# Kernel optimization log

Measured on AMD Instinct MI355X. Metric: run time of the kernel, lower is better.

## Reference

```python
import jax, jax.numpy as jnp
import numpy as np

MESSAGE_PASSES = 3  # constants.message_passes
F_NODE = 64   # hidden_node_features
F_EDGE = 16   # n_edge_features
M_MSG = 64    # message_size
OUT_DIM = 128
B, N = 8, 256
EDGE_DENSITY = 0.1


def setup_inputs() -> dict:
    key = jax.random.key(0)
    ks = jax.random.split(key, 12)
    nodes = jax.random.normal(ks[0], (B, N, F_NODE), dtype=jnp.float32)
    # sparse positive edge features: rand * bernoulli connectivity (avg degree ~ N*density)
    raw = jax.random.uniform(ks[1], (B, N, N, F_EDGE), dtype=jnp.float32)
    conn = (jax.random.uniform(ks[2], (B, N, N)) < EDGE_DENSITY).astype(jnp.float32)
    edges = raw * conn[..., None]
    s = 0.05
    return {
        "nodes": nodes,
        "edges": edges,
        # message MLP: cat(neighbour, edge) -> message_size
        "W_msg": jax.random.normal(ks[3], (F_NODE + F_EDGE, M_MSG), dtype=jnp.float32) * s,
        "b_msg": jnp.zeros((M_MSG,), dtype=jnp.float32),
        # GRU cell (input=message_size, hidden=F_NODE), gates [r|z|n]
        "W_i": jax.random.normal(ks[4], (M_MSG, 3 * F_NODE), dtype=jnp.float32) * s,
        "W_h": jax.random.normal(ks[5], (F_NODE, 3 * F_NODE), dtype=jnp.float32) * s,
        "b_i": jnp.zeros((3 * F_NODE,), dtype=jnp.float32),
        "b_h": jnp.zeros((3 * F_NODE,), dtype=jnp.float32),
        # gated readout
        "W_g": jax.random.normal(ks[6], (2 * F_NODE, OUT_DIM), dtype=jnp.float32) * s,
        "b_g": jnp.zeros((OUT_DIM,), dtype=jnp.float32),
        "W_e": jax.random.normal(ks[7], (F_NODE, OUT_DIM), dtype=jnp.float32) * s,
        "b_e": jnp.zeros((OUT_DIM,), dtype=jnp.float32),
    }


def reference(nodes, edges, W_msg, b_msg, W_i, W_h, b_i, b_h, W_g, b_g, W_e, b_e):
    # adjacency[b,i,j] != 0  <=>  edge (i<-j) exists (original: edges.sum(3).nonzero)
    adjacency = edges.sum(axis=-1)                                   # (B,N,N)
    nbr_mask = (adjacency != 0).astype(nodes.dtype)                  # (B,N,N)
    node_mask = (adjacency.sum(axis=-1) != 0)                        # (B,N) bool
    node_mask_f = node_mask.astype(nodes.dtype)

    h = nodes                                                        # hidden_nodes init = nodes
    b, n, f = nodes.shape
    for _ in range(MESSAGE_PASSES):
        # message_terms over all (node i, neighbour j) pairs; masked sum == padded-gather sum
        nghb = jnp.broadcast_to(h[:, None, :, :], (b, n, n, f))      # (B,N,N,F) neighbour feats
        feat = jnp.concatenate([nghb, edges], axis=-1)               # (B,N,N,F+E)
        terms = jax.nn.relu(feat @ W_msg + b_msg)                    # (B,N,N,M)
        messages = jnp.einsum('bijm,bij->bim', terms, nbr_mask)      # summation aggregation
        # GRU cell update
        gi = messages @ W_i + b_i                                    # (B,N,3F)
        gh = h @ W_h + b_h
        ir, iz, inn = jnp.split(gi, 3, axis=-1)
        hr, hz, hn = jnp.split(gh, 3, axis=-1)
        r = jax.nn.sigmoid(ir + hr)
        z = jax.nn.sigmoid(iz + hz)
        ng = jnp.tanh(inn + r * hn)
        h_new = (1.0 - z) * ng + z * h
        # only nodes with nonzero degree are scattered back (original indexes node_batch idc)
        h = jnp.where(node_mask[..., None], h_new, h)

    # gated readout: sum_i mask_i * sigmoid(g([h_i, x_i])) * e(h_i)
    gate = jax.nn.sigmoid(jnp.concatenate([h, nodes], axis=-1) @ W_g + b_g)  # (B,N,OUT)
    emb = h @ W_e + b_e                                                      # (B,N,OUT)
    out = jnp.einsum('bno,bn->bo', gate * emb, node_mask_f)                  # (B,OUT)
    return out
```

## Files before the change

kernel.cpp:

```cpp
#include <hip/hip_runtime.h>
#include <hip/hip_bf16.h>

#define BB 8
#define NN 256
#define FF 64
#define EE 16
#define MM 64
#define G3 192
#define OUTD 128
#define ROWS (BB*NN)
#define MAXD 64

__global__ __launch_bounds__(256) void k_prep(
    const float* __restrict__ nodes, const float* __restrict__ edges,
    const float* __restrict__ Wmsg, const float* __restrict__ bmsg,
    int* __restrict__ deg, int* __restrict__ nbr,
    float* __restrict__ h, float* __restrict__ hn)
{
    int row = blockIdx.x;
    int tid = threadIdx.x;
    __shared__ int cnt;
    __shared__ float snode[FF];
    if (tid == 0) cnt = 0;
    __syncthreads();

    const float4* ep = (const float4*)(edges + (((size_t)row) * NN + tid) * EE);
    float4 a = ep[0], b4 = ep[1], c4 = ep[2], d4 = ep[3];
    float s = a.x + a.y + a.z + a.w + b4.x + b4.y + b4.z + b4.w
            + c4.x + c4.y + c4.z + c4.w + d4.x + d4.y + d4.z + d4.w;
    if (s != 0.0f) {
        int slot = atomicAdd(&cnt, 1);
        if (slot < MAXD) nbr[row * MAXD + slot] = tid;
    }
    if (tid < FF) snode[tid] = nodes[(size_t)row * FF + tid];
    __syncthreads();

    if (tid == 0) deg[row] = (cnt < MAXD) ? cnt : MAXD;
    if (tid < FF) h[row * FF + tid] = snode[tid];
    if (tid < MM) {
        float acc = bmsg[tid];
        #pragma unroll 8
        for (int k = 0; k < FF; ++k) acc += snode[k] * Wmsg[k * MM + tid];
        hn[row * MM + tid] = acc;
    }
}

#define MSG_WAVES 4
__global__ __launch_bounds__(256) void k_msg(
    const float* __restrict__ edges, const float* __restrict__ Wmsg,
    const int* __restrict__ deg, const int* __restrict__ nbr,
    const float* __restrict__ hn, float* __restrict__ msg)
{
    int row = blockIdx.x;
    int b   = row >> 8;
    int tid = threadIdx.x;
    int w   = tid >> 6;
    int t   = tid & 63;

    float we[EE];
    #pragma unroll
    for (int k = 0; k < EE; ++k) we[k] = Wmsg[(FF + k) * MM + t];

    __shared__ float efeat[MAXD][EE];
    __shared__ float part[MSG_WAVES][MM];

    int d = deg[row];
    for (int s4 = tid; s4 < d * EE; s4 += 256) {
        int slot = s4 >> 4, k = s4 & 15;
        int j = nbr[row * MAXD + slot];
        efeat[slot][k] = edges[(((size_t)row) * NN + j) * EE + k];
    }
    __syncthreads();

    float acc = 0.0f;
    for (int s = w; s < d; s += MSG_WAVES) {
        int j = nbr[row * MAXD + s];
        float term = hn[(((size_t)b) * NN + j) * MM + t];
        #pragma unroll
        for (int k = 0; k < EE; ++k) term += efeat[s][k] * we[k];
        acc += fmaxf(term, 0.0f);
    }
    part[w][t] = acc;
    __syncthreads();
    if (w == 0) {
        msg[row * MM + t] = part[0][t] + part[1][t] + part[2][t] + part[3][t];
    }
}

#define GRU_NODES 8
__global__ __launch_bounds__(512) void k_gru(
    const float* __restrict__ Wi, const float* __restrict__ Wh,
    const float* __restrict__ bi, const float* __restrict__ bh,
    const float* __restrict__ Wmsg, const float* __restrict__ bmsg,
    const int* __restrict__ deg,
    const float* __restrict__ msg, float* __restrict__ h, float* __restrict__ hn,
    int last)
{
    int g = threadIdx.x >> 6;
    int t = threadIdx.x & 63;
    int row = blockIdx.x * GRU_NODES + g;

    __shared__ float sm[GRU_NODES][FF];
    __shared__ float sh[GRU_NODES][FF];
    sm[g][t] = msg[row * MM + t];
    sh[g][t] = h[row * FF + t];
    __syncthreads();

    float ir = bi[t], iz = bi[64 + t], in_ = bi[128 + t];
    float hr = bh[t], hz = bh[64 + t], hn_ = bh[128 + t];
    #pragma unroll 4
    for (int k = 0; k < FF; ++k) {
        float mk = sm[g][k], hk = sh[g][k];
        ir  += mk * Wi[k * G3 + t];
        iz  += mk * Wi[k * G3 + 64 + t];
        in_ += mk * Wi[k * G3 + 128 + t];
        hr  += hk * Wh[k * G3 + t];
        hz  += hk * Wh[k * G3 + 64 + t];
        hn_ += hk * Wh[k * G3 + 128 + t];
    }
    float r  = 1.0f / (1.0f + __expf(-(ir + hr)));
    float z  = 1.0f / (1.0f + __expf(-(iz + hz)));
    float ng = tanhf(in_ + r * hn_);
    float hold = sh[g][t];
    float hnew = (1.0f - z) * ng + z * hold;
    if (deg[row] == 0) hnew = hold;
    h[row * FF + t] = hnew;

    __syncthreads();
    sh[g][t] = hnew;
    __syncthreads();

    if (!last) {
        float acc = bmsg[t];
        #pragma unroll 8
        for (int k = 0; k < FF; ++k) acc += sh[g][k] * Wmsg[k * MM + t];
        hn[row * MM + t] = acc;
    }
}

#define RO_NODES 8
__global__ __launch_bounds__(1024) void k_readout(
    const float* __restrict__ nodes, const float* __restrict__ Wg,
    const float* __restrict__ bg, const float* __restrict__ We,
    const float* __restrict__ be, const int* __restrict__ deg,
    const float* __restrict__ h, float* __restrict__ out)
{
    int g = threadIdx.x >> 7;
    int o = threadIdx.x & 127;
    int row = blockIdx.x * RO_NODES + g;
    int b   = row >> 8;

    __shared__ float sh[RO_NODES][FF];
    __shared__ float sx[RO_NODES][FF];
    __shared__ float red[RO_NODES][OUTD];
    if (o < FF) {
        sh[g][o] = h[row * FF + o];
        sx[g][o] = nodes[(size_t)row * FF + o];
    }
    __syncthreads();

    float gacc = bg[o], eacc = be[o];
    #pragma unroll 4
    for (int k = 0; k < FF; ++k) {
        float hk = sh[g][k];
        gacc += hk * Wg[k * OUTD + o];
        eacc += hk * We[k * OUTD + o];
    }
    #pragma unroll 4
    for (int k = 0; k < FF; ++k) gacc += sx[g][k] * Wg[(FF + k) * OUTD + o];

    float val = (deg[row] != 0) ? (1.0f / (1.0f + __expf(-gacc))) * eacc : 0.0f;
    red[g][o] = val;
    __syncthreads();
    if (g == 0) {
        float s = 0.0f;
        #pragma unroll
        for (int q = 0; q < RO_NODES; ++q) s += red[q][o];
        atomicAdd(&out[b * OUTD + o], s);
    }
}

extern "C" void kernel_launch(void* const* d_in, const int* in_sizes, int n_in,
                              void* d_out, int out_size, void* d_ws, size_t ws_size,
                              hipStream_t stream) {
    const float* nodes = (const float*)d_in[0];
    const float* edges = (const float*)d_in[1];
    const float* Wmsg  = (const float*)d_in[2];
    const float* bmsg  = (const float*)d_in[3];
    const float* Wi    = (const float*)d_in[4];
    const float* Wh    = (const float*)d_in[5];
    const float* bi    = (const float*)d_in[6];
    const float* bh    = (const float*)d_in[7];
    const float* Wg    = (const float*)d_in[8];
    const float* bg    = (const float*)d_in[9];
    const float* We    = (const float*)d_in[10];
    const float* be    = (const float*)d_in[11];
    float* out = (float*)d_out;

    char* ws = (char*)d_ws;
    int*   deg = (int*)ws;
    int*   nbr = (int*)(ws + 8192);
    float* h   = (float*)(ws + 8192 + ROWS * MAXD * 4);
    float* hn  = h + ROWS * FF;
    float* msg = hn + ROWS * MM;

    hipMemsetAsync(d_out, 0, (size_t)BB * OUTD * sizeof(float), stream);

    k_prep<<<ROWS, 256, 0, stream>>>(nodes, edges, Wmsg, bmsg, deg, nbr, h, hn);

    for (int p = 0; p < 3; ++p) {
        k_msg<<<ROWS, 256, 0, stream>>>(edges, Wmsg, deg, nbr, hn, msg);
        k_gru<<<ROWS / GRU_NODES, 64 * GRU_NODES, 0, stream>>>(
            Wi, Wh, bi, bh, Wmsg, bmsg, deg, msg, h, hn, (p == 2) ? 1 : 0);
    }

    k_readout<<<ROWS / RO_NODES, 128 * RO_NODES, 0, stream>>>(
        nodes, Wg, bg, We, be, deg, h, out);
}
```

Measured before the change: 166.8 us.

## Fuse message, GRU, projection and readout into one per-pass kernel

Merges the message aggregation, GRU update, next-pass neighbour projection and, on the last pass, the gated readout into a single kernel per pass, with one block per node. This cuts the launch count from eight to four, removes the msg round trip through global memory, and ping-pongs hn between two buffers to avoid read/write hazards across nodes. The neighbour-list build now uses wave ballot and popcount instead of shared atomics, which also makes the neighbour order deterministic. In exchange, the GRU and readout math run one node per block, so the weight matrices are reloaded per node and only part of each 256-thread block is busy during those phases.

```diff
diff --git a/kernel.cpp b/kernel.cpp
--- a/kernel.cpp
+++ b/kernel.cpp
@@ -11,6 +11,10 @@
 #define ROWS (BB*NN)
 #define MAXD 64
 
+__device__ __forceinline__ float sigmoidf_(float x) {
+    return 1.0f / (1.0f + __expf(-x));
+}
+
 __global__ __launch_bounds__(256) void k_prep(
     const float* __restrict__ nodes, const float* __restrict__ edges,
     const float* __restrict__ Wmsg, const float* __restrict__ bmsg,
@@ -19,23 +23,30 @@
 {
     int row = blockIdx.x;
     int tid = threadIdx.x;
-    __shared__ int cnt;
+    int lane = tid & 63, wv = tid >> 6;
+    __shared__ int wcnt[4];
     __shared__ float snode[FF];
-    if (tid == 0) cnt = 0;
-    __syncthreads();
 
     const float4* ep = (const float4*)(edges + (((size_t)row) * NN + tid) * EE);
     float4 a = ep[0], b4 = ep[1], c4 = ep[2], d4 = ep[3];
     float s = a.x + a.y + a.z + a.w + b4.x + b4.y + b4.z + b4.w
             + c4.x + c4.y + c4.z + c4.w + d4.x + d4.y + d4.z + d4.w;
-    if (s != 0.0f) {
-        int slot = atomicAdd(&cnt, 1);
-        if (slot < MAXD) nbr[row * MAXD + slot] = tid;
-    }
+    bool pred = (s != 0.0f);
+    unsigned long long m = __ballot(pred);
+    if (lane == 0) wcnt[wv] = __popcll(m);
     if (tid < FF) snode[tid] = nodes[(size_t)row * FF + tid];
     __syncthreads();
 
-    if (tid == 0) deg[row] = (cnt < MAXD) ? cnt : MAXD;
+    int base = 0;
+    #pragma unroll
+    for (int q = 0; q < 4; ++q) base += (q < wv) ? wcnt[q] : 0;
+    int slot = base + __popcll(m & ((1ull << lane) - 1ull));
+    if (pred && slot < MAXD) nbr[row * MAXD + slot] = tid;
+
+    if (tid == 0) {
+        int tot = wcnt[0] + wcnt[1] + wcnt[2] + wcnt[3];
+        deg[row] = (tot < MAXD) ? tot : MAXD;
+    }
     if (tid < FF) h[row * FF + tid] = snode[tid];
     if (tid < MM) {
         float acc = bmsg[tid];
@@ -45,138 +56,115 @@
     }
 }
 
-#define MSG_WAVES 4
-__global__ __launch_bounds__(256) void k_msg(
-    const float* __restrict__ edges, const float* __restrict__ Wmsg,
+__global__ __launch_bounds__(256) void k_pass(
+    const float* __restrict__ edges,
+    const float* __restrict__ Wmsg, const float* __restrict__ bmsg,
+    const float* __restrict__ Wi, const float* __restrict__ Wh,
+    const float* __restrict__ bi, const float* __restrict__ bh,
+    const float* __restrict__ nodes,
+    const float* __restrict__ Wg, const float* __restrict__ bg,
+    const float* __restrict__ We, const float* __restrict__ be,
     const int* __restrict__ deg, const int* __restrict__ nbr,
-    const float* __restrict__ hn, float* __restrict__ msg)
+    const float* __restrict__ hn_in, float* __restrict__ hn_out,
+    float* __restrict__ h, float* __restrict__ out, int last)
 {
-    int row = blockIdx.x;
-    int b   = row >> 8;
+    int row = blockIdx.x, b = row >> 8;
     int tid = threadIdx.x;
-    int w   = tid >> 6;
-    int t   = tid & 63;
+    int w = tid >> 6, t = tid & 63;
+
+    __shared__ int   snbr[MAXD];
+    __shared__ float efeat[MAXD][EE];
+    __shared__ float part[4][MM];
+    __shared__ float smsg[MM];
+    __shared__ float shold[FF];
+    __shared__ float sx[FF];
+    __shared__ float gI[3][FF], gH[3][FF];
+    __shared__ float shnew[FF];
+    __shared__ float eo[OUTD];
+
+    int d = deg[row];
+    if (tid < d)  snbr[tid]  = nbr[row * MAXD + tid];
+    if (tid < FF) shold[tid] = h[row * FF + tid];
+    if (last && tid < FF) sx[tid] = nodes[(size_t)row * FF + tid];
 
     float we[EE];
     #pragma unroll
     for (int k = 0; k < EE; ++k) we[k] = Wmsg[(FF + k) * MM + t];
-
-    __shared__ float efeat[MAXD][EE];
-    __shared__ float part[MSG_WAVES][MM];
-
-    int d = deg[row];
+    __syncthreads();
+
     for (int s4 = tid; s4 < d * EE; s4 += 256) {
         int slot = s4 >> 4, k = s4 & 15;
-        int j = nbr[row * MAXD + slot];
-        efeat[slot][k] = edges[(((size_t)row) * NN + j) * EE + k];
+        efeat[slot][k] = edges[(((size_t)row) * NN + snbr[slot]) * EE + k];
     }
     __syncthreads();
 
     float acc = 0.0f;
-    for (int s = w; s < d; s += MSG_WAVES) {
-        int j = nbr[row * MAXD + s];
-        float term = hn[(((size_t)b) * NN + j) * MM + t];
+    for (int s = w; s < d; s += 4) {
+        int j = snbr[s];
+        float term = hn_in[(((size_t)b) * NN + j) * MM + t];
         #pragma unroll
         for (int k = 0; k < EE; ++k) term += efeat[s][k] * we[k];
         acc += fmaxf(term, 0.0f);
     }
     part[w][t] = acc;
     __syncthreads();
+    if (w == 0) smsg[t] = part[0][t] + part[1][t] + part[2][t] + part[3][t];
+    __syncthreads();
+
+    if (w < 3) {
+        float gi = bi[w * FF + t], gh = bh[w * FF + t];
+        #pragma unroll 4
+        for (int k = 0; k < FF; ++k) {
+            gi += smsg[k]  * Wi[k * G3 + w * FF + t];
+            gh += shold[k] * Wh[k * G3 + w * FF + t];
+        }
+        gI[w][t] = gi; gH[w][t] = gh;
+    }
+    __syncthreads();
+
     if (w == 0) {
-        msg[row * MM + t] = part[0][t] + part[1][t] + part[2][t] + part[3][t];
-    }
-}
-
-#define GRU_NODES 8
-__global__ __launch_bounds__(512) void k_gru(
-    const float* __restrict__ Wi, const float* __restrict__ Wh,
-    const float* __restrict__ bi, const float* __restrict__ bh,
-    const float* __restrict__ Wmsg, const float* __restrict__ bmsg,
-    const int* __restrict__ deg,
-    const float* __restrict__ msg, float* __restrict__ h, float* __restrict__ hn,
-    int last)
-{
-    int g = threadIdx.x >> 6;
-    int t = threadIdx.x & 63;
-    int row = blockIdx.x * GRU_NODES + g;
-
-    __shared__ float sm[GRU_NODES][FF];
-    __shared__ float sh[GRU_NODES][FF];
-    sm[g][t] = msg[row * MM + t];
-    sh[g][t] = h[row * FF + t];
-    __syncthreads();
-
-    float ir = bi[t], iz = bi[64 + t], in_ = bi[128 + t];
-    float hr = bh[t], hz = bh[64 + t], hn_ = bh[128 + t];
-    #pragma unroll 4
-    for (int k = 0; k < FF; ++k) {
-        float mk = sm[g][k], hk = sh[g][k];
-        ir  += mk * Wi[k * G3 + t];
-        iz  += mk * Wi[k * G3 + 64 + t];
-        in_ += mk * Wi[k * G3 + 128 + t];
-        hr  += hk * Wh[k * G3 + t];
-        hz  += hk * Wh[k * G3 + 64 + t];
-        hn_ += hk * Wh[k * G3 + 128 + t];
-    }
-    float r  = 1.0f / (1.0f + __expf(-(ir + hr)));
-    float z  = 1.0f / (1.0f + __expf(-(iz + hz)));
-    float ng = tanhf(in_ + r * hn_);
-    float hold = sh[g][t];
-    float hnew = (1.0f - z) * ng + z * hold;
-    if (deg[row] == 0) hnew = hold;
-    h[row * FF + t] = hnew;
-
-    __syncthreads();
-    sh[g][t] = hnew;
+        float r  = sigmoidf_(gI[0][t] + gH[0][t]);
+        float z  = sigmoidf_(gI[1][t] + gH[1][t]);
+        float ng = tanhf(gI[2][t] + r * gH[2][t]);
+        float hold = shold[t];
+        float hnew = (1.0f - z) * ng + z * hold;
+        if (d == 0) hnew = hold;
+        shnew[t] = hnew;
+        h[row * FF + t] = hnew;
+    }
     __syncthreads();
 
     if (!last) {
-        float acc = bmsg[t];
-        #pragma unroll 8
-        for (int k = 0; k < FF; ++k) acc += sh[g][k] * Wmsg[k * MM + t];
-        hn[row * MM + t] = acc;
-    }
-}
-
-#define RO_NODES 8
-__global__ __launch_bounds__(1024) void k_readout(
-    const float* __restrict__ nodes, const float* __restrict__ Wg,
-    const float* __restrict__ bg, const float* __restrict__ We,
-    const float* __restrict__ be, const int* __restrict__ deg,
-    const float* __restrict__ h, float* __restrict__ out)
-{
-    int g = threadIdx.x >> 7;
-    int o = threadIdx.x & 127;
-    int row = blockIdx.x * RO_NODES + g;
-    int b   = row >> 8;
-
-    __shared__ float sh[RO_NODES][FF];
-    __shared__ float sx[RO_NODES][FF];
-    __shared__ float red[RO_NODES][OUTD];
-    if (o < FF) {
-        sh[g][o] = h[row * FF + o];
-        sx[g][o] = nodes[(size_t)row * FF + o];
-    }
-    __syncthreads();
-
-    float gacc = bg[o], eacc = be[o];
-    #pragma unroll 4
-    for (int k = 0; k < FF; ++k) {
-        float hk = sh[g][k];
-        gacc += hk * Wg[k * OUTD + o];
-        eacc += hk * We[k * OUTD + o];
-    }
-    #pragma unroll 4
-    for (int k = 0; k < FF; ++k) gacc += sx[g][k] * Wg[(FF + k) * OUTD + o];
-
-    float val = (deg[row] != 0) ? (1.0f / (1.0f + __expf(-gacc))) * eacc : 0.0f;
-    red[g][o] = val;
-    __syncthreads();
-    if (g == 0) {
-        float s = 0.0f;
+        float p = 0.0f;
         #pragma unroll
-        for (int q = 0; q < RO_NODES; ++q) s += red[q][o];
-        atomicAdd(&out[b * OUTD + o], s);
+        for (int kk = 0; kk < 16; ++kk) {
+            int k = w * 16 + kk;
+            p += shnew[k] * Wmsg[k * MM + t];
+        }
+        part[w][t] = p;
+        __syncthreads();
+        if (w == 0)
+            hn_out[row * MM + t] = bmsg[t] + part[0][t] + part[1][t] + part[2][t] + part[3][t];
+    } else {
+        int o = tid & 127, half = tid >> 7;
+        float g = 0.0f;
+        if (half == 1) {
+            float e = be[o];
+            #pragma unroll 4
+            for (int k = 0; k < FF; ++k) e += shnew[k] * We[k * OUTD + o];
+            eo[o] = e;
+        } else {
+            g = bg[o];
+            #pragma unroll 4
+            for (int k = 0; k < FF; ++k) g += shnew[k] * Wg[k * OUTD + o];
+            #pragma unroll 4
+            for (int k = 0; k < FF; ++k) g += sx[k] * Wg[(FF + k) * OUTD + o];
+        }
+        __syncthreads();
+        if (half == 0 && d != 0) {
+            float val = sigmoidf_(g) * eo[o];
+            atomicAdd(&out[b * OUTD + o], val);
+        }
     }
 }
 
@@ -198,22 +186,23 @@
     float* out = (float*)d_out;
 
     char* ws = (char*)d_ws;
-    int*   deg = (int*)ws;
-    int*   nbr = (int*)(ws + 8192);
-    float* h   = (float*)(ws + 8192 + ROWS * MAXD * 4);
-    float* hn  = h + ROWS * FF;
-    float* msg = hn + ROWS * MM;
+    int*   deg  = (int*)ws;
+    int*   nbr  = (int*)(ws + 8192);
+    float* h    = (float*)(ws + 8192 + ROWS * MAXD * 4);
+    float* hnA  = h   + ROWS * FF;
+    float* hnB  = hnA + ROWS * MM;
 
     hipMemsetAsync(d_out, 0, (size_t)BB * OUTD * sizeof(float), stream);
 
-    k_prep<<<ROWS, 256, 0, stream>>>(nodes, edges, Wmsg, bmsg, deg, nbr, h, hn);
-
-    for (int p = 0; p < 3; ++p) {
-        k_msg<<<ROWS, 256, 0, stream>>>(edges, Wmsg, deg, nbr, hn, msg);
-        k_gru<<<ROWS / GRU_NODES, 64 * GRU_NODES, 0, stream>>>(
-            Wi, Wh, bi, bh, Wmsg, bmsg, deg, msg, h, hn, (p == 2) ? 1 : 0);
-    }
-
-    k_readout<<<ROWS / RO_NODES, 128 * RO_NODES, 0, stream>>>(
-        nodes, Wg, bg, We, be, deg, h, out);
-}
+    k_prep<<<ROWS, 256, 0, stream>>>(nodes, edges, Wmsg, bmsg, deg, nbr, h, hnA);
+
+    k_pass<<<ROWS, 256, 0, stream>>>(edges, Wmsg, bmsg, Wi, Wh, bi, bh,
+                                     nodes, Wg, bg, We, be, deg, nbr,
+                                     hnA, hnB, h, out, 0);
+    k_pass<<<ROWS, 256, 0, stream>>>(edges, Wmsg, bmsg, Wi, Wh, bi, bh,
+                                     nodes, Wg, bg, We, be, deg, nbr,
+                                     hnB, hnA, h, out, 0);
+    k_pass<<<ROWS, 256, 0, stream>>>(edges, Wmsg, bmsg, Wi, Wh, bi, bh,
+                                     nodes, Wg, bg, We, be, deg, nbr,
+                                     hnA, hnB, h, out, 1);
+}
```

After: 156.2 us. 1.07x faster.
